# Optimization experiments

Hardware: AMD Instinct MI355X
Metric: run time of the kernel (lower is better)

The kernel has to match this reference:

```python
import jax, jax.numpy as jnp
import numpy as np

B, H, W, C = 4, 64, 64, 1280
NH = 16          # num heads
HD = C // NH     # 80 features per head
WS = 14          # window size
REL = 2 * WS - 1 # 27 relative-position entries per axis
EPS = 1e-6


def setup_inputs() -> dict:
    key = jax.random.key(0)
    ks = jax.random.split(key, 16)
    s = 0.02
    return {
        "imagelike_bhwc": jax.random.normal(ks[0], (B, H, W, C), jnp.float32),
        "ln1_g": jnp.ones((C,), jnp.float32),
        "ln1_b": jnp.zeros((C,), jnp.float32),
        "qkv_w": jax.random.normal(ks[1], (C, 3 * C), jnp.float32) * s,
        "qkv_b": jnp.zeros((3 * C,), jnp.float32),
        "proj_w": jax.random.normal(ks[2], (C, C), jnp.float32) * s,
        "proj_b": jnp.zeros((C,), jnp.float32),
        "rel_pos_h": jax.random.normal(ks[3], (REL, HD), jnp.float32) * s,
        "rel_pos_w": jax.random.normal(ks[4], (REL, HD), jnp.float32) * s,
        "ln2_g": jnp.ones((C,), jnp.float32),
        "ln2_b": jnp.zeros((C,), jnp.float32),
        "mlp_w1": jax.random.normal(ks[5], (C, 4 * C), jnp.float32) * s,
        "mlp_b1": jnp.zeros((4 * C,), jnp.float32),
        "mlp_w2": jax.random.normal(ks[6], (4 * C, C), jnp.float32) * s,
        "mlp_b2": jnp.zeros((C,), jnp.float32),
    }


def _layernorm(t, g, b):
    mu = jnp.mean(t, axis=-1, keepdims=True)
    var = jnp.var(t, axis=-1, keepdims=True)
    return (t - mu) * jax.lax.rsqrt(var + EPS) * g + b


def reference(imagelike_bhwc, ln1_g, ln1_b, qkv_w, qkv_b, proj_w, proj_b,
              rel_pos_h, rel_pos_w, ln2_g, ln2_b, mlp_w1, mlp_b1, mlp_w2, mlp_b2):
    x = imagelike_bhwc
    b, h, w, c = x.shape
    hd = c // NH
    scale = hd ** -0.5
    # --- image -> windows (pad to multiple of WS) ---
    hp, wp = (-h) % WS, (-w) % WS
    xp = jnp.pad(x, ((0, 0), (0, hp), (0, wp), (0, 0)))
    Hp, Wp = h + hp, w + wp
    ny, nx = Hp // WS, Wp // WS
    win = xp.reshape(b, ny, WS, nx, WS, c).transpose(0, 1, 3, 2, 4, 5)
    win = win.reshape(b * ny * nx, WS, WS, c)      # (Bw, S, S, C)
    Bw, N = win.shape[0], WS * WS
    # --- pre-attention layernorm + qkv ---
    t = _layernorm(win, ln1_g, ln1_b)
    qkv = t.reshape(Bw, N, c) @ qkv_w + qkv_b      # (Bw, N, 3C)
    qkv = qkv.reshape(Bw, N, 3, NH, hd).transpose(2, 0, 3, 1, 4)  # (3,Bw,NH,N,hd)
    q, k, v = qkv[0], qkv[1], qkv[2]
    # --- scores + decomposed relative position bias ---
    attn = jnp.einsum('bhqd,bhkd->bhqk', q * scale, k)            # (Bw,NH,N,N)
    idx = jnp.arange(WS)[:, None] - jnp.arange(WS)[None, :] + (WS - 1)
    Rh = rel_pos_h[idx]                                           # (WS,WS,hd)
    Rw = rel_pos_w[idx]                                           # (WS,WS,hd)
    qr = q.reshape(Bw, NH, WS, WS, hd)
    bias_h = jnp.einsum('bnyxd,ykd->bnyxk', qr, Rh)               # (Bw,NH,WS,WS,WS)
    bias_w = jnp.einsum('bnyxd,xkd->bnyxk', qr, Rw)
    bias = (bias_h[..., :, None] + bias_w[..., None, :]).reshape(Bw, NH, N, N)
    attn = jax.nn.softmax(attn + bias, axis=-1)
    out = jnp.einsum('bhqk,bhkd->bhqd', attn, v)                  # (Bw,NH,N,hd)
    out = out.transpose(0, 2, 1, 3).reshape(Bw, WS, WS, c)
    out = out @ proj_w + proj_b
    attn_out = out + win                                          # residual 1
    # --- MLP ---
    t2 = _layernorm(attn_out, ln2_g, ln2_b)
    mlp = jax.nn.gelu(t2 @ mlp_w1 + mlp_b1, approximate=False) @ mlp_w2 + mlp_b2
    out = mlp + attn_out                                          # residual 2
    # --- windows -> image (remove padding) ---
    img = out.reshape(b, ny, nx, WS, WS, c).transpose(0, 1, 3, 2, 4, 5)
    img = img.reshape(b, Hp, Wp, c)
    return img[:, :h, :w, :]
```

## Files before the change

kernel.cpp:

```cpp
#include <hip/hip_runtime.h>

typedef __attribute__((ext_vector_type(8))) short short8;
typedef __attribute__((ext_vector_type(4))) float f32x4;

#define GLBP(p) ((const __attribute__((address_space(1))) void*)(p))
#define LDSP(p) ((__attribute__((address_space(3))) void*)(p))

__device__ __forceinline__ float bf2f(unsigned short u) {
  return __uint_as_float(((unsigned int)u) << 16);
}
__device__ __forceinline__ unsigned short f2bf(float f) {
  unsigned int u = __float_as_uint(f);
  u += 0x7fff + ((u >> 16) & 1);
  return (unsigned short)(u >> 16);
}

__device__ __forceinline__ void tok2pix(int gt, int& b, int& py, int& px) {
  int w = gt / 196, t = gt - w * 196;
  b = w / 25;
  int wr = w - b * 25;
  int wy = wr / 5, wx = wr - wy * 5;
  int ty = t / 14;
  py = wy * 14 + ty;
  px = wx * 14 + (t - ty * 14);
}

__global__ void k_transpose(const float* __restrict__ W, unsigned short* __restrict__ Wt,
                            int K, int N) {
  __shared__ float tile[32][33];
  int tx = threadIdx.x, ty = threadIdx.y;
  int n0 = blockIdx.x * 32, k0 = blockIdx.y * 32;
#pragma unroll
  for (int i = 0; i < 4; ++i)
    tile[ty + 8 * i][tx] = W[(size_t)(k0 + ty + 8 * i) * N + n0 + tx];
  __syncthreads();
#pragma unroll
  for (int i = 0; i < 4; ++i)
    Wt[(size_t)(n0 + ty + 8 * i) * K + k0 + tx] = f2bf(tile[tx][ty + 8 * i]);
}

__global__ __launch_bounds__(256) void k_ln1(const float* __restrict__ x,
                                             const float* __restrict__ g,
                                             const float* __restrict__ be,
                                             unsigned short* __restrict__ A1,
                                             int w0, int ctok) {
  int m = blockIdx.x * 4 + (threadIdx.x >> 6);
  int lane = threadIdx.x & 63;
  int b, py, px;
  tok2pix(w0 * 196 + m, b, py, px);
  bool valid = (m < ctok) && (py < 64) && (px < 64);
  const float* row = x + ((size_t)((b * 64 + py) * 64 + px)) * 1280;
  float v[20];
#pragma unroll
  for (int i = 0; i < 20; ++i) v[i] = valid ? row[lane + 64 * i] : 0.f;
  float s = 0.f, ss = 0.f;
#pragma unroll
  for (int i = 0; i < 20; ++i) { s += v[i]; ss += v[i] * v[i]; }
#pragma unroll
  for (int o = 32; o > 0; o >>= 1) { s += __shfl_down(s, o); ss += __shfl_down(ss, o); }
  s = __shfl(s, 0);
  ss = __shfl(ss, 0);
  float mu = s * (1.f / 1280.f);
  float var = ss * (1.f / 1280.f) - mu * mu;
  float rinv = rsqrtf(var + 1e-6f);
  unsigned short* o1 = A1 + (size_t)m * 1280;
#pragma unroll
  for (int i = 0; i < 20; ++i) {
    int c = lane + 64 * i;
    o1[c] = f2bf((v[i] - mu) * rinv * g[c] + be[c]);
  }
}

__global__ __launch_bounds__(256) void k_ln2(const unsigned short* __restrict__ AT,
                                             const float* __restrict__ g,
                                             const float* __restrict__ be,
                                             unsigned short* __restrict__ A2) {
  int m = blockIdx.x * 4 + (threadIdx.x >> 6);
  int lane = threadIdx.x & 63;
  const unsigned short* row = AT + (size_t)m * 1280;
  float v[20];
#pragma unroll
  for (int i = 0; i < 20; ++i) v[i] = bf2f(row[lane + 64 * i]);
  float s = 0.f, ss = 0.f;
#pragma unroll
  for (int i = 0; i < 20; ++i) { s += v[i]; ss += v[i] * v[i]; }
#pragma unroll
  for (int o = 32; o > 0; o >>= 1) { s += __shfl_down(s, o); ss += __shfl_down(ss, o); }
  s = __shfl(s, 0);
  ss = __shfl(ss, 0);
  float mu = s * (1.f / 1280.f);
  float var = ss * (1.f / 1280.f) - mu * mu;
  float rinv = rsqrtf(var + 1e-6f);
  unsigned short* o1 = A2 + (size_t)m * 1280;
#pragma unroll
  for (int i = 0; i < 20; ++i) {
    int c = lane + 64 * i;
    o1[c] = f2bf((v[i] - mu) * rinv * g[c] + be[c]);
  }
}

template <int EPI>
__device__ __forceinline__ void gemm_body(const unsigned short* __restrict__ A,
                                          const unsigned short* __restrict__ Bt,
                                          int K, int N, int gx,
                                          const float* __restrict__ bias,
                                          void* __restrict__ outp,
                                          const float* __restrict__ xres,
                                          const unsigned short* __restrict__ attnres,
                                          int w0, int ctok) {
  __shared__ __align__(16) char smem[147456];
  int tid = threadIdx.x;
  int w = tid >> 6, lane = tid & 63;
  int nwg = gridDim.x, bid = blockIdx.x;
  int q = nwg >> 3, r = nwg & 7;
  int xcd = bid & 7, loc = bid >> 3;
  int wg = (xcd < r ? xcd * (q + 1) : r * (q + 1) + (xcd - r) * q) + loc;
  int bx = wg % gx, by = wg / gx;
  int mBase = by * 256, nBase = bx * 128;
  int wr = w >> 2, wc = w & 3;
  int la = lane & 15, lg = lane >> 4;

  int srow = tid >> 3;
  int ssw = ((tid & 7) * 16) ^ ((srow & 7) << 4);
  const char* pa[4];
  const char* pb[2];
#pragma unroll
  for (int i = 0; i < 4; ++i)
    pa[i] = (const char*)A + ((size_t)(mBase + srow + i * 64) * K) * 2 + ssw;
#pragma unroll
  for (int i = 0; i < 2; ++i)
    pb[i] = (const char*)Bt + ((size_t)(nBase + srow + i * 64) * K) * 2 + ssw;
  int ldst = tid * 16;

  auto STAGE = [&](int sb, size_t ko) {
#pragma unroll
    for (int i = 0; i < 4; ++i)
      __builtin_amdgcn_global_load_lds(GLBP(pa[i] + ko), LDSP(smem + sb + i * 8192 + ldst), 16, 0, 0);
#pragma unroll
    for (int i = 0; i < 2; ++i)
      __builtin_amdgcn_global_load_lds(GLBP(pb[i] + ko), LDSP(smem + sb + 32768 + i * 8192 + ldst), 16, 0, 0);
  };

  int colk[2];
#pragma unroll
  for (int kk = 0; kk < 2; ++kk) colk[kk] = (kk * 64 + lg * 16) ^ ((la & 7) << 4);
  int offA[8];
#pragma unroll
  for (int m = 0; m < 8; ++m) offA[m] = (wr * 128 + m * 16 + la) * 128;
  int offB[2];
#pragma unroll
  for (int n = 0; n < 2; ++n) offB[n] = 32768 + (wc * 32 + n * 16 + la) * 128;

  const f32x4 z4 = {0.f, 0.f, 0.f, 0.f};
  f32x4 acc[8][2];
#pragma unroll
  for (int m = 0; m < 8; ++m)
#pragma unroll
    for (int n = 0; n < 2; ++n) acc[m][n] = z4;

  int NT = K >> 6;
  STAGE(0, 0);
  STAGE(49152, 128);
  int rs = 0;
  for (int t = 0; t < NT; ++t) {
    if (t + 1 < NT)
      asm volatile("s_waitcnt vmcnt(6)" ::: "memory");
    else
      asm volatile("s_waitcnt vmcnt(0)" ::: "memory");
    __builtin_amdgcn_s_barrier();
    __builtin_amdgcn_sched_barrier(0);
    const char* buf = (const char*)smem + rs * 49152;
    if (t + 2 < NT) {
      int ws = rs + 2;
      if (ws >= 3) ws -= 3;
      STAGE(ws * 49152, (size_t)(t + 2) * 128);
    }
    short8 bfr[2][2], af[4][2];
#pragma unroll
    for (int n = 0; n < 2; ++n)
#pragma unroll
      for (int kk = 0; kk < 2; ++kk) bfr[n][kk] = *(const short8*)(buf + offB[n] + colk[kk]);
#pragma unroll
    for (int m = 0; m < 4; ++m)
#pragma unroll
      for (int kk = 0; kk < 2; ++kk) af[m][kk] = *(const short8*)(buf + offA[m] + colk[kk]);
    __builtin_amdgcn_s_setprio(1);
#pragma unroll
    for (int m = 0; m < 4; ++m)
#pragma unroll
      for (int n = 0; n < 2; ++n)
#pragma unroll
        for (int kk = 0; kk < 2; ++kk)
          acc[m][n] = __builtin_amdgcn_mfma_f32_16x16x32_bf16(af[m][kk], bfr[n][kk], acc[m][n], 0, 0, 0);
    __builtin_amdgcn_s_setprio(0);
    __builtin_amdgcn_sched_barrier(0);
#pragma unroll
    for (int m = 0; m < 4; ++m)
#pragma unroll
      for (int kk = 0; kk < 2; ++kk) af[m][kk] = *(const short8*)(buf + offA[m + 4] + colk[kk]);
    __builtin_amdgcn_s_setprio(1);
#pragma unroll
    for (int m = 0; m < 4; ++m)
#pragma unroll
      for (int n = 0; n < 2; ++n)
#pragma unroll
        for (int kk = 0; kk < 2; ++kk)
          acc[m + 4][n] = __builtin_amdgcn_mfma_f32_16x16x32_bf16(af[m][kk], bfr[n][kk], acc[m + 4][n], 0, 0, 0);
    __builtin_amdgcn_s_setprio(0);
    rs = (rs == 2) ? 0 : rs + 1;
  }

#pragma unroll
  for (int m = 0; m < 8; ++m) {
#pragma unroll
    for (int n = 0; n < 2; ++n) {
      int col = nBase + wc * 32 + n * 16 + la;
      float bcol = bias[col];
#pragma unroll
      for (int j = 0; j < 4; ++j) {
        int row = mBase + wr * 128 + m * 16 + lg * 4 + j;
        float v = acc[m][n][j] + bcol;
        if (EPI == 0) {
          ((unsigned short*)outp)[(size_t)row * N + col] = f2bf(v);
        } else if (EPI == 2) {
          float gg = 0.5f * v * (1.f + erff(v * 0.70710678118654752f));
          ((unsigned short*)outp)[(size_t)row * N + col] = f2bf(gg);
        } else if (EPI == 1) {
          if (row < ctok) {
            int b, py, px;
            tok2pix(w0 * 196 + row, b, py, px);
            float wv = (py < 64 && px < 64)
                           ? xres[((size_t)((b * 64 + py) * 64 + px)) * 1280 + col]
                           : 0.f;
            ((unsigned short*)outp)[(size_t)row * 1280 + col] = f2bf(v + wv);
          }
        } else {
          if (row < ctok) {
            int b, py, px;
            tok2pix(w0 * 196 + row, b, py, px);
            if (py < 64 && px < 64)
              ((float*)outp)[((size_t)((b * 64 + py) * 64 + px)) * 1280 + col] =
                  v + bf2f(attnres[(size_t)row * 1280 + col]);
          }
        }
      }
    }
  }
}

__global__ __launch_bounds__(512, 2) void k_gqkv(const unsigned short* A, const unsigned short* Bt,
                                                 int K, int N, int gx, const float* bias, void* o,
                                                 const float* xr, const unsigned short* ar, int w0, int ct) {
  gemm_body<0>(A, Bt, K, N, gx, bias, o, xr, ar, w0, ct);
}
__global__ __launch_bounds__(512, 2) void k_gproj(const unsigned short* A, const unsigned short* Bt,
                                                  int K, int N, int gx, const float* bias, void* o,
                                                  const float* xr, const unsigned short* ar, int w0, int ct) {
  gemm_body<1>(A, Bt, K, N, gx, bias, o, xr, ar, w0, ct);
}
__global__ __launch_bounds__(512, 2) void k_gmlp1(const unsigned short* A, const unsigned short* Bt,
                                                  int K, int N, int gx, const float* bias, void* o,
                                                  const float* xr, const unsigned short* ar, int w0, int ct) {
  gemm_body<2>(A, Bt, K, N, gx, bias, o, xr, ar, w0, ct);
}
__global__ __launch_bounds__(512, 2) void k_gmlp2(const unsigned short* A, const unsigned short* Bt,
                                                  int K, int N, int gx, const float* bias, void* o,
                                                  const float* xr, const unsigned short* ar, int w0, int ct) {
  gemm_body<3>(A, Bt, K, N, gx, bias, o, xr, ar, w0, ct);
}

__global__ __launch_bounds__(256) void k_relbias(const unsigned short* __restrict__ qkv,
                                                 const float* __restrict__ rph,
                                                 const float* __restrict__ rpw,
                                                 unsigned short* __restrict__ B) {
  int wh = blockIdx.x;
  int w = wh >> 4, nh = wh & 15;
  const unsigned short* qb = qkv + (size_t)w * 196 * 3840 + nh * 80;
  for (int id = threadIdx.x; id < 196 * 28; id += 256) {
    int t = id / 28, which = id - t * 28;
    int y = t / 14, xx = t - y * 14;
    const float* R = (which < 14) ? (rph + (size_t)(y - which + 13) * 80)
                                  : (rpw + (size_t)(xx - (which - 14) + 13) * 80);
    const unsigned short* qq = qb + (size_t)t * 3840;
    float acc = 0.f;
#pragma unroll
    for (int d8 = 0; d8 < 10; ++d8) {
      short8 qv = *(const short8*)(qq + d8 * 8);
      const float4* Rv = (const float4*)(R + d8 * 8);
      float4 ra = Rv[0], rb = Rv[1];
      acc += bf2f((unsigned short)qv[0]) * ra.x + bf2f((unsigned short)qv[1]) * ra.y +
             bf2f((unsigned short)qv[2]) * ra.z + bf2f((unsigned short)qv[3]) * ra.w +
             bf2f((unsigned short)qv[4]) * rb.x + bf2f((unsigned short)qv[5]) * rb.y +
             bf2f((unsigned short)qv[6]) * rb.z + bf2f((unsigned short)qv[7]) * rb.w;
    }
    B[(size_t)wh * (196 * 28) + id] = f2bf(acc);
  }
}

__global__ __launch_bounds__(512) void k_attn(const unsigned short* __restrict__ qkv,
                                              const unsigned short* __restrict__ Bias,
                                              unsigned short* __restrict__ AO) {
  __shared__ unsigned short Ks[208 * 104];
  __shared__ unsigned short Vt[80 * 248];
  __shared__ unsigned short Ps[8][16 * 248];
  __shared__ unsigned short Bls[196 * 28];
  int wh = blockIdx.x;
  int w = wh >> 4, nh = wh & 15;
  int tid = threadIdx.x, wid = tid >> 6, lane = tid & 63;
  int la = lane & 15, lg = lane >> 4;
  const unsigned short* base = qkv + (size_t)w * 196 * 3840 + nh * 80;
  const short8 z8 = {0, 0, 0, 0, 0, 0, 0, 0};

  for (int c = tid; c < 208 * 13; c += 512) {
    int t = c / 13, seg = c - t * 13;
    short8 kv = z8;
    if (t < 196 && seg < 10) kv = *(const short8*)(base + (size_t)t * 3840 + 1280 + seg * 8);
    *(short8*)(Ks + t * 104 + seg * 8) = kv;
  }
  for (int c = tid; c < 196 * 10; c += 512) {
    int t = c / 10, d8 = (c - t * 10) * 8;
    short8 vv = *(const short8*)(base + (size_t)t * 3840 + 2560 + d8);
#pragma unroll
    for (int e = 0; e < 8; ++e) Vt[(d8 + e) * 248 + t] = (unsigned short)vv[e];
  }
  for (int i = tid; i < 80 * 28; i += 512) Vt[(i / 28) * 248 + 196 + (i % 28)] = 0;
  for (int i = tid; i < 196 * 28; i += 512) Bls[i] = Bias[(size_t)wh * (196 * 28) + i];
  __syncthreads();

  int kyv[13], kxv[13];
#pragma unroll
  for (int ci = 0; ci < 13; ++ci) {
    int key = ci * 16 + la;
    kyv[ci] = key / 14;
    kxv[ci] = key - kyv[ci] * 14;
  }

  const float scale = 0.111803398874989485f;
  const f32x4 z4 = {0.f, 0.f, 0.f, 0.f};
  unsigned short* P = Ps[wid];

  auto process = [&](int rb) {
    short8 qa[3];
#pragma unroll
    for (int kk = 0; kk < 3; ++kk) {
      int t = rb * 16 + la;
      int d = kk * 32 + lg * 8;
      qa[kk] = (t < 196 && d < 80) ? *(const short8*)(base + (size_t)t * 3840 + d) : z8;
    }
    f32x4 s[13];
#pragma unroll
    for (int i = 0; i < 13; ++i) s[i] = z4;
#pragma unroll
    for (int kk = 0; kk < 3; ++kk) {
#pragma unroll
      for (int ni = 0; ni < 13; ++ni) {
        short8 bb = *(const short8*)(Ks + (ni * 16 + la) * 104 + kk * 32 + lg * 8);
        s[ni] = __builtin_amdgcn_mfma_f32_16x16x32_bf16(qa[kk], bb, s[ni], 0, 0, 0);
      }
    }
#pragma unroll
    for (int j = 0; j < 4; ++j) {
      int rloc = lg * 4 + j;
      int t = rb * 16 + rloc;
      bool tval = t < 196;
      const unsigned short* Bp = Bls + (tval ? t : 0) * 28;
      float v[13];
      float mx = -3e30f;
#pragma unroll
      for (int ci = 0; ci < 13; ++ci) {
        int key = ci * 16 + la;
        float val = s[ci][j] * scale;
        if (key < 196 && tval) val += bf2f(Bp[kyv[ci]]) + bf2f(Bp[14 + kxv[ci]]);
        if (key >= 196) val = -3e30f;
        v[ci] = val;
        mx = fmaxf(mx, val);
      }
#pragma unroll
      for (int o = 1; o < 16; o <<= 1) mx = fmaxf(mx, __shfl_xor(mx, o));
      float sum = 0.f;
#pragma unroll
      for (int ci = 0; ci < 13; ++ci) {
        float e = __expf(v[ci] - mx);
        v[ci] = e;
        sum += e;
      }
#pragma unroll
      for (int o = 1; o < 16; o <<= 1) sum += __shfl_xor(sum, o);
      float inv = 1.f / sum;
#pragma unroll
      for (int ci = 0; ci < 13; ++ci) P[rloc * 248 + ci * 16 + la] = f2bf(v[ci] * inv);
      P[rloc * 248 + 208 + la] = 0;
    }
    f32x4 o5[5];
#pragma unroll
    for (int i = 0; i < 5; ++i) o5[i] = z4;
#pragma unroll
    for (int kc = 0; kc < 7; ++kc) {
      short8 a = *(const short8*)(P + la * 248 + kc * 32 + lg * 8);
#pragma unroll
      for (int ni = 0; ni < 5; ++ni) {
        short8 bb = *(const short8*)(Vt + (ni * 16 + la) * 248 + kc * 32 + lg * 8);
        o5[ni] = __builtin_amdgcn_mfma_f32_16x16x32_bf16(a, bb, o5[ni], 0, 0, 0);
      }
    }
#pragma unroll
    for (int ni = 0; ni < 5; ++ni)
#pragma unroll
      for (int j = 0; j < 4; ++j) {
        int t = rb * 16 + lg * 4 + j;
        if (t < 196)
          AO[((size_t)w * 196 + t) * 1280 + nh * 80 + ni * 16 + la] = f2bf(o5[ni][j]);
      }
  };

  process(wid);
  if (wid < 5) process(wid + 8);
}

extern "C" void kernel_launch(void* const* d_in, const int* in_sizes, int n_in,
                              void* d_out, int out_size, void* d_ws, size_t ws_size,
                              hipStream_t stream) {
  const float* x = (const float*)d_in[0];
  const float* ln1g = (const float*)d_in[1];
  const float* ln1b = (const float*)d_in[2];
  const float* qkvw = (const float*)d_in[3];
  const float* qkvb = (const float*)d_in[4];
  const float* projw = (const float*)d_in[5];
  const float* projb = (const float*)d_in[6];
  const float* rph = (const float*)d_in[7];
  const float* rpw = (const float*)d_in[8];
  const float* ln2g = (const float*)d_in[9];
  const float* ln2b = (const float*)d_in[10];
  const float* w1 = (const float*)d_in[11];
  const float* b1 = (const float*)d_in[12];
  const float* w2 = (const float*)d_in[13];
  const float* b2 = (const float*)d_in[14];
  float* out = (float*)d_out;

  const size_t woff = (3840ull * 1280 + 1280ull * 1280 + 5120ull * 1280 + 1280ull * 5120) * 2;
  const int NWopts[7] = {100, 50, 25, 10, 5, 2, 1};
  int NW = 0, Mb = 0;
  for (int i = 0; i < 7; ++i) {
    int nw = NWopts[i];
    int mb = ((nw * 196 + 255) / 256) * 256;
    size_t tot = woff + (size_t)mb * 2560  + (size_t)mb * 7680  +
                 (size_t)mb * 2560  + (size_t)nw * 16 * 196 * 28 * 2  +
                 (size_t)mb * 2560 ;
    if (tot <= ws_size) { NW = nw; Mb = mb; break; }
  }
  if (!NW) return;

  char* p = (char*)d_ws;
  unsigned short* qkvwT = (unsigned short*)p; p += 3840ull * 1280 * 2;
  unsigned short* projwT = (unsigned short*)p; p += 1280ull * 1280 * 2;
  unsigned short* w1T = (unsigned short*)p; p += 5120ull * 1280 * 2;
  unsigned short* w2T = (unsigned short*)p; p += 1280ull * 5120 * 2;
  unsigned short* A1 = (unsigned short*)p; p += (size_t)Mb * 2560;
  unsigned short* QKV = (unsigned short*)p; p += (size_t)Mb * 7680;
  unsigned short* AO = (unsigned short*)p; p += (size_t)Mb * 2560;
  unsigned short* BIAS = (unsigned short*)p; p += (size_t)NW * 16 * 196 * 28 * 2;
  unsigned short* ATTN = (unsigned short*)p;
  unsigned short* Hb = QKV;
  unsigned short* A2 = A1;

  k_transpose<<<dim3(120, 40), dim3(32, 8), 0, stream>>>(qkvw, qkvwT, 1280, 3840);
  k_transpose<<<dim3(40, 40), dim3(32, 8), 0, stream>>>(projw, projwT, 1280, 1280);
  k_transpose<<<dim3(160, 40), dim3(32, 8), 0, stream>>>(w1, w1T, 1280, 5120);
  k_transpose<<<dim3(40, 160), dim3(32, 8), 0, stream>>>(w2, w2T, 5120, 1280);

  int gy = Mb / 256;
  int nchunks = (100 + NW - 1) / NW;
  for (int c = 0; c < nchunks; ++c) {
    int w0 = c * NW;
    int cw = (100 - w0 < NW) ? (100 - w0) : NW;
    int ctok = cw * 196;
    k_ln1<<<Mb / 4, 256, 0, stream>>>(x, ln1g, ln1b, A1, w0, ctok);
    k_gqkv<<<30 * gy, 512, 0, stream>>>(A1, qkvwT, 1280, 3840, 30, qkvb, (void*)QKV,
                                        nullptr, nullptr, 0, 0);
    k_relbias<<<cw * 16, 256, 0, stream>>>(QKV, rph, rpw, BIAS);
    k_attn<<<cw * 16, 512, 0, stream>>>(QKV, BIAS, AO);
    k_gproj<<<10 * gy, 512, 0, stream>>>(AO, projwT, 1280, 1280, 10, projb, (void*)ATTN,
                                         x, nullptr, w0, ctok);
    k_ln2<<<Mb / 4, 256, 0, stream>>>(ATTN, ln2g, ln2b, A2);
    k_gmlp1<<<40 * gy, 512, 0, stream>>>(A2, w1T, 1280, 5120, 40, b1, (void*)Hb,
                                         nullptr, nullptr, 0, 0);
    k_gmlp2<<<10 * gy, 512, 0, stream>>>(Hb, w2T, 5120, 1280, 10, b2, (void*)out,
                                         nullptr, ATTN, w0, ctok);
  }
}
```

Measured before the change: 1.808 ms.

## Halve GEMM K-tile for higher occupancy, fuse relbias into attention, per-head QKV layout

The GEMM K step drops from 64 to 32, which cuts the LDS ring from 144KB to 72KB, with a new XOR swizzle and launch bounds raised to 4 blocks per CU. The QKV GEMM epilogue now writes Q/K/V in a per-window, per-head contiguous layout, so attention reads contiguous rows. The separate relative-position bias kernel and its workspace buffer are removed, and the bias is computed inside the attention kernel. Attention blocks are remapped so the 8 windows sharing a head are adjacent. This trades more barriers per K and possible register pressure for better occupancy and less traffic.

```diff
diff --git a/kernel.cpp b/kernel.cpp
--- a/kernel.cpp
+++ b/kernel.cpp
@@ -108,7 +108,7 @@
                                           const float* __restrict__ xres,
                                           const unsigned short* __restrict__ attnres,
                                           int w0, int ctok) {
-  __shared__ __align__(16) char smem[147456];
+  __shared__ __align__(16) char smem[73728];
   int tid = threadIdx.x;
   int w = tid >> 6, lane = tid & 63;
   int nwg = gridDim.x, bid = blockIdx.x;
@@ -120,36 +120,31 @@
   int wr = w >> 2, wc = w & 3;
   int la = lane & 15, lg = lane >> 4;
 
-  int srow = tid >> 3;
-  int ssw = ((tid & 7) * 16) ^ ((srow & 7) << 4);
-  const char* pa[4];
-  const char* pb[2];
-#pragma unroll
-  for (int i = 0; i < 4; ++i)
-    pa[i] = (const char*)A + ((size_t)(mBase + srow + i * 64) * K) * 2 + ssw;
-#pragma unroll
-  for (int i = 0; i < 2; ++i)
-    pb[i] = (const char*)Bt + ((size_t)(nBase + srow + i * 64) * K) * 2 + ssw;
+  int srow = tid >> 2;
+  int schunk = (tid & 3) ^ ((srow >> 1) & 3);
+  const char* pa0 = (const char*)A + (size_t)(mBase + srow) * K * 2 + (schunk << 4);
+  const char* pa1 = (const char*)A + (size_t)(mBase + 128 + srow) * K * 2 + (schunk << 4);
+  const char* pb0 = (const char*)Bt + (size_t)(nBase + srow) * K * 2 + (schunk << 4);
   int ldst = tid * 16;
 
-  auto STAGE = [&](int sb, size_t ko) {
-#pragma unroll
-    for (int i = 0; i < 4; ++i)
-      __builtin_amdgcn_global_load_lds(GLBP(pa[i] + ko), LDSP(smem + sb + i * 8192 + ldst), 16, 0, 0);
-#pragma unroll
-    for (int i = 0; i < 2; ++i)
-      __builtin_amdgcn_global_load_lds(GLBP(pb[i] + ko), LDSP(smem + sb + 32768 + i * 8192 + ldst), 16, 0, 0);
+  auto STAGE = [&](int slot, size_t ko) {
+    int b = slot * 24576;
+    __builtin_amdgcn_global_load_lds(GLBP(pa0 + ko), LDSP(smem + b + ldst), 16, 0, 0);
+    __builtin_amdgcn_global_load_lds(GLBP(pa1 + ko), LDSP(smem + b + 8192 + ldst), 16, 0, 0);
+    __builtin_amdgcn_global_load_lds(GLBP(pb0 + ko), LDSP(smem + b + 16384 + ldst), 16, 0, 0);
   };
 
-  int colk[2];
-#pragma unroll
-  for (int kk = 0; kk < 2; ++kk) colk[kk] = (kk * 64 + lg * 16) ^ ((la & 7) << 4);
-  int offA[8];
-#pragma unroll
-  for (int m = 0; m < 8; ++m) offA[m] = (wr * 128 + m * 16 + la) * 128;
-  int offB[2];
-#pragma unroll
-  for (int n = 0; n < 2; ++n) offB[n] = 32768 + (wc * 32 + n * 16 + la) * 128;
+  int offA[8], offB[2];
+#pragma unroll
+  for (int m = 0; m < 8; ++m) {
+    int rr = wr * 128 + m * 16 + la;
+    offA[m] = rr * 64 + ((lg ^ ((rr >> 1) & 3)) << 4);
+  }
+#pragma unroll
+  for (int n = 0; n < 2; ++n) {
+    int rr = wc * 32 + n * 16 + la;
+    offB[n] = 16384 + rr * 64 + ((lg ^ ((rr >> 1) & 3)) << 4);
+  }
 
   const f32x4 z4 = {0.f, 0.f, 0.f, 0.f};
   f32x4 acc[8][2];
@@ -158,54 +153,44 @@
 #pragma unroll
     for (int n = 0; n < 2; ++n) acc[m][n] = z4;
 
-  int NT = K >> 6;
+  int NT = K >> 5;
   STAGE(0, 0);
-  STAGE(49152, 128);
+  STAGE(1, 64);
   int rs = 0;
   for (int t = 0; t < NT; ++t) {
     if (t + 1 < NT)
-      asm volatile("s_waitcnt vmcnt(6)" ::: "memory");
+      asm volatile("s_waitcnt vmcnt(3)" ::: "memory");
     else
       asm volatile("s_waitcnt vmcnt(0)" ::: "memory");
     __builtin_amdgcn_s_barrier();
     __builtin_amdgcn_sched_barrier(0);
-    const char* buf = (const char*)smem + rs * 49152;
     if (t + 2 < NT) {
       int ws = rs + 2;
       if (ws >= 3) ws -= 3;
-      STAGE(ws * 49152, (size_t)(t + 2) * 128);
-    }
-    short8 bfr[2][2], af[4][2];
-#pragma unroll
-    for (int n = 0; n < 2; ++n)
-#pragma unroll
-      for (int kk = 0; kk < 2; ++kk) bfr[n][kk] = *(const short8*)(buf + offB[n] + colk[kk]);
+      STAGE(ws, (size_t)(t + 2) * 64);
+    }
+    const char* buf = (const char*)smem + rs * 24576;
+    short8 af[4], bfr[2];
+#pragma unroll
+    for (int n = 0; n < 2; ++n) bfr[n] = *(const short8*)(buf + offB[n]);
+#pragma unroll
+    for (int m = 0; m < 4; ++m) af[m] = *(const short8*)(buf + offA[m]);
+    __builtin_amdgcn_s_setprio(1);
 #pragma unroll
     for (int m = 0; m < 4; ++m)
 #pragma unroll
-      for (int kk = 0; kk < 2; ++kk) af[m][kk] = *(const short8*)(buf + offA[m] + colk[kk]);
-    __builtin_amdgcn_s_setprio(1);
-#pragma unroll
-    for (int m = 0; m < 4; ++m)
-#pragma unroll
       for (int n = 0; n < 2; ++n)
-#pragma unroll
-        for (int kk = 0; kk < 2; ++kk)
-          acc[m][n] = __builtin_amdgcn_mfma_f32_16x16x32_bf16(af[m][kk], bfr[n][kk], acc[m][n], 0, 0, 0);
+        acc[m][n] = __builtin_amdgcn_mfma_f32_16x16x32_bf16(af[m], bfr[n], acc[m][n], 0, 0, 0);
     __builtin_amdgcn_s_setprio(0);
     __builtin_amdgcn_sched_barrier(0);
 #pragma unroll
+    for (int m = 0; m < 4; ++m) af[m] = *(const short8*)(buf + offA[m + 4]);
+    __builtin_amdgcn_s_setprio(1);
+#pragma unroll
     for (int m = 0; m < 4; ++m)
 #pragma unroll
-      for (int kk = 0; kk < 2; ++kk) af[m][kk] = *(const short8*)(buf + offA[m + 4] + colk[kk]);
-    __builtin_amdgcn_s_setprio(1);
-#pragma unroll
-    for (int m = 0; m < 4; ++m)
-#pragma unroll
       for (int n = 0; n < 2; ++n)
-#pragma unroll
-        for (int kk = 0; kk < 2; ++kk)
-          acc[m + 4][n] = __builtin_amdgcn_mfma_f32_16x16x32_bf16(af[m][kk], bfr[n][kk], acc[m + 4][n], 0, 0, 0);
+        acc[m + 4][n] = __builtin_amdgcn_mfma_f32_16x16x32_bf16(af[m], bfr[n], acc[m + 4][n], 0, 0, 0);
     __builtin_amdgcn_s_setprio(0);
     rs = (rs == 2) ? 0 : rs + 1;
   }
@@ -221,7 +206,13 @@
         int row = mBase + wr * 128 + m * 16 + lg * 4 + j;
         float v = acc[m][n][j] + bcol;
         if (EPI == 0) {
-          ((unsigned short*)outp)[(size_t)row * N + col] = f2bf(v);
+          if (row < ctok) {
+            int wloc = row / 196, tt = row - wloc * 196;
+            int which = col / 1280, cr = col - which * 1280;
+            int nh = cr / 80, d = cr - nh * 80;
+            ((unsigned short*)outp)[((((size_t)wloc * 16 + nh) * 3 + which) * 196 + tt) * 80 + d] =
+                f2bf(v);
+          }
         } else if (EPI == 2) {
           float gg = 0.5f * v * (1.f + erff(v * 0.70710678118654752f));
           ((unsigned short*)outp)[(size_t)row * N + col] = f2bf(gg);
@@ -248,40 +239,66 @@
   }
 }
 
-__global__ __launch_bounds__(512, 2) void k_gqkv(const unsigned short* A, const unsigned short* Bt,
+__global__ __launch_bounds__(512, 4) void k_gqkv(const unsigned short* A, const unsigned short* Bt,
                                                  int K, int N, int gx, const float* bias, void* o,
                                                  const float* xr, const unsigned short* ar, int w0, int ct) {
   gemm_body<0>(A, Bt, K, N, gx, bias, o, xr, ar, w0, ct);
 }
-__global__ __launch_bounds__(512, 2) void k_gproj(const unsigned short* A, const unsigned short* Bt,
+__global__ __launch_bounds__(512, 4) void k_gproj(const unsigned short* A, const unsigned short* Bt,
                                                   int K, int N, int gx, const float* bias, void* o,
                                                   const float* xr, const unsigned short* ar, int w0, int ct) {
   gemm_body<1>(A, Bt, K, N, gx, bias, o, xr, ar, w0, ct);
 }
-__global__ __launch_bounds__(512, 2) void k_gmlp1(const unsigned short* A, const unsigned short* Bt,
+__global__ __launch_bounds__(512, 4) void k_gmlp1(const unsigned short* A, const unsigned short* Bt,
                                                   int K, int N, int gx, const float* bias, void* o,
                                                   const float* xr, const unsigned short* ar, int w0, int ct) {
   gemm_body<2>(A, Bt, K, N, gx, bias, o, xr, ar, w0, ct);
 }
-__global__ __launch_bounds__(512, 2) void k_gmlp2(const unsigned short* A, const unsigned short* Bt,
+__global__ __launch_bounds__(512, 4) void k_gmlp2(const unsigned short* A, const unsigned short* Bt,
                                                   int K, int N, int gx, const float* bias, void* o,
                                                   const float* xr, const unsigned short* ar, int w0, int ct) {
   gemm_body<3>(A, Bt, K, N, gx, bias, o, xr, ar, w0, ct);
 }
 
-__global__ __launch_bounds__(256) void k_relbias(const unsigned short* __restrict__ qkv,
-                                                 const float* __restrict__ rph,
-                                                 const float* __restrict__ rpw,
-                                                 unsigned short* __restrict__ B) {
-  int wh = blockIdx.x;
-  int w = wh >> 4, nh = wh & 15;
-  const unsigned short* qb = qkv + (size_t)w * 196 * 3840 + nh * 80;
-  for (int id = threadIdx.x; id < 196 * 28; id += 256) {
-    int t = id / 28, which = id - t * 28;
+__global__ __launch_bounds__(512) void k_attn(const unsigned short* __restrict__ qkv,
+                                              const float* __restrict__ rph,
+                                              const float* __restrict__ rpw,
+                                              unsigned short* __restrict__ AO, int cw) {
+  int bid = blockIdx.x;
+  int r = bid & 7, nh = (bid >> 3) & 15, a = bid >> 7;
+  int w = 8 * a + r;
+  if (w >= cw) return;
+
+  __shared__ unsigned short Ks[208 * 104];
+  __shared__ unsigned short Vt[80 * 248];
+  __shared__ unsigned short Ps[8][16 * 248];
+  __shared__ unsigned short Bls[196 * 28];
+  int tid = threadIdx.x, wid = tid >> 6, lane = tid & 63;
+  int la = lane & 15, lg = lane >> 4;
+  const unsigned short* qb = qkv + ((size_t)(w * 16 + nh)) * 3 * 15680;
+  const unsigned short* kb = qb + 15680;
+  const unsigned short* vb = qb + 31360;
+  const short8 z8 = {0, 0, 0, 0, 0, 0, 0, 0};
+
+  for (int c = tid; c < 208 * 13; c += 512) {
+    int t = c / 13, seg = c - t * 13;
+    short8 kv = z8;
+    if (t < 196 && seg < 10) kv = *(const short8*)(kb + (size_t)t * 80 + seg * 8);
+    *(short8*)(Ks + t * 104 + seg * 8) = kv;
+  }
+  for (int c = tid; c < 196 * 10; c += 512) {
+    int t = c / 10, d8 = (c - t * 10) * 8;
+    short8 vv = *(const short8*)(vb + (size_t)t * 80 + d8);
+#pragma unroll
+    for (int e = 0; e < 8; ++e) Vt[(d8 + e) * 248 + t] = (unsigned short)vv[e];
+  }
+  for (int i = tid; i < 80 * 52; i += 512) Vt[(i / 52) * 248 + 196 + (i % 52)] = 0;
+  for (int id = tid; id < 196 * 28; id += 512) {
+    int t = id / 28, c = id - t * 28;
     int y = t / 14, xx = t - y * 14;
-    const float* R = (which < 14) ? (rph + (size_t)(y - which + 13) * 80)
-                                  : (rpw + (size_t)(xx - (which - 14) + 13) * 80);
-    const unsigned short* qq = qb + (size_t)t * 3840;
+    const float* R = (c < 14) ? (rph + (size_t)(y - c + 13) * 80)
+                              : (rpw + (size_t)(xx - (c - 14) + 13) * 80);
+    const unsigned short* qq = qb + (size_t)t * 80;
     float acc = 0.f;
 #pragma unroll
     for (int d8 = 0; d8 < 10; ++d8) {
@@ -293,38 +310,8 @@
              bf2f((unsigned short)qv[4]) * rb.x + bf2f((unsigned short)qv[5]) * rb.y +
              bf2f((unsigned short)qv[6]) * rb.z + bf2f((unsigned short)qv[7]) * rb.w;
     }
-    B[(size_t)wh * (196 * 28) + id] = f2bf(acc);
-  }
-}
-
-__global__ __launch_bounds__(512) void k_attn(const unsigned short* __restrict__ qkv,
-                                              const unsigned short* __restrict__ Bias,
-                                              unsigned short* __restrict__ AO) {
-  __shared__ unsigned short Ks[208 * 104];
-  __shared__ unsigned short Vt[80 * 248];
-  __shared__ unsigned short Ps[8][16 * 248];
-  __shared__ unsigned short Bls[196 * 28];
-  int wh = blockIdx.x;
-  int w = wh >> 4, nh = wh & 15;
-  int tid = threadIdx.x, wid = tid >> 6, lane = tid & 63;
-  int la = lane & 15, lg = lane >> 4;
-  const unsigned short* base = qkv + (size_t)w * 196 * 3840 + nh * 80;
-  const short8 z8 = {0, 0, 0, 0, 0, 0, 0, 0};
-
-  for (int c = tid; c < 208 * 13; c += 512) {
-    int t = c / 13, seg = c - t * 13;
-    short8 kv = z8;
-    if (t < 196 && seg < 10) kv = *(const short8*)(base + (size_t)t * 3840 + 1280 + seg * 8);
-    *(short8*)(Ks + t * 104 + seg * 8) = kv;
-  }
-  for (int c = tid; c < 196 * 10; c += 512) {
-    int t = c / 10, d8 = (c - t * 10) * 8;
-    short8 vv = *(const short8*)(base + (size_t)t * 3840 + 2560 + d8);
-#pragma unroll
-    for (int e = 0; e < 8; ++e) Vt[(d8 + e) * 248 + t] = (unsigned short)vv[e];
-  }
-  for (int i = tid; i < 80 * 28; i += 512) Vt[(i / 28) * 248 + 196 + (i % 28)] = 0;
-  for (int i = tid; i < 196 * 28; i += 512) Bls[i] = Bias[(size_t)wh * (196 * 28) + i];
+    Bls[id] = f2bf(acc);
+  }
   __syncthreads();
 
   int kyv[13], kxv[13];
@@ -345,7 +332,7 @@
     for (int kk = 0; kk < 3; ++kk) {
       int t = rb * 16 + la;
       int d = kk * 32 + lg * 8;
-      qa[kk] = (t < 196 && d < 80) ? *(const short8*)(base + (size_t)t * 3840 + d) : z8;
+      qa[kk] = (t < 196 && d < 80) ? *(const short8*)(qb + (size_t)t * 80 + d) : z8;
     }
     f32x4 s[13];
 #pragma unroll
@@ -396,11 +383,11 @@
     for (int i = 0; i < 5; ++i) o5[i] = z4;
 #pragma unroll
     for (int kc = 0; kc < 7; ++kc) {
-      short8 a = *(const short8*)(P + la * 248 + kc * 32 + lg * 8);
+      short8 aa = *(const short8*)(P + la * 248 + kc * 32 + lg * 8);
 #pragma unroll
       for (int ni = 0; ni < 5; ++ni) {
         short8 bb = *(const short8*)(Vt + (ni * 16 + la) * 248 + kc * 32 + lg * 8);
-        o5[ni] = __builtin_amdgcn_mfma_f32_16x16x32_bf16(a, bb, o5[ni], 0, 0, 0);
+        o5[ni] = __builtin_amdgcn_mfma_f32_16x16x32_bf16(aa, bb, o5[ni], 0, 0, 0);
       }
     }
 #pragma unroll
@@ -444,8 +431,7 @@
     int nw = NWopts[i];
     int mb = ((nw * 196 + 255) / 256) * 256;
     size_t tot = woff + (size_t)mb * 2560  + (size_t)mb * 7680  +
-                 (size_t)mb * 2560  + (size_t)nw * 16 * 196 * 28 * 2  +
-                 (size_t)mb * 2560 ;
+                 (size_t)mb * 2560  + (size_t)mb * 2560 ;
     if (tot <= ws_size) { NW = nw; Mb = mb; break; }
   }
   if (!NW) return;
@@ -458,7 +444,6 @@
   unsigned short* A1 = (unsigned short*)p; p += (size_t)Mb * 2560;
   unsigned short* QKV = (unsigned short*)p; p += (size_t)Mb * 7680;
   unsigned short* AO = (unsigned short*)p; p += (size_t)Mb * 2560;
-  unsigned short* BIAS = (unsigned short*)p; p += (size_t)NW * 16 * 196 * 28 * 2;
   unsigned short* ATTN = (unsigned short*)p;
   unsigned short* Hb = QKV;
   unsigned short* A2 = A1;
@@ -476,14 +461,14 @@
     int ctok = cw * 196;
     k_ln1<<<Mb / 4, 256, 0, stream>>>(x, ln1g, ln1b, A1, w0, ctok);
     k_gqkv<<<30 * gy, 512, 0, stream>>>(A1, qkvwT, 1280, 3840, 30, qkvb, (void*)QKV,
-                                        nullptr, nullptr, 0, 0);
-    k_relbias<<<cw * 16, 256, 0, stream>>>(QKV, rph, rpw, BIAS);
-    k_attn<<<cw * 16, 512, 0, stream>>>(QKV, BIAS, AO);
+                                        nullptr, nullptr, 0, ctok);
+    int ablk = ((cw + 7) / 8) * 128;
+    k_attn<<<ablk, 512, 0, stream>>>(QKV, rph, rpw, AO, cw);
     k_gproj<<<10 * gy, 512, 0, stream>>>(AO, projwT, 1280, 1280, 10, projb, (void*)ATTN,
                                          x, nullptr, w0, ctok);
     k_ln2<<<Mb / 4, 256, 0, stream>>>(ATTN, ln2g, ln2b, A2);
     k_gmlp1<<<40 * gy, 512, 0, stream>>>(A2, w1T, 1280, 5120, 40, b1, (void*)Hb,
-                                         nullptr, nullptr, 0, 0);
+                                         nullptr, nullptr, 0, ctok);
     k_gmlp2<<<10 * gy, 512, 0, stream>>>(Hb, w2T, 5120, 1280, 10, b2, (void*)out,
                                          nullptr, ATTN, w0, ctok);
   }
```

Measured after the change: 1.603 ms. 11.3% less time.
